# Kernel tuning notes

Hardware: AMD Instinct MI355X
Metric: run time of the kernel (lower is better)

The kernel has to match this reference:

```python
import jax, jax.numpy as jnp
import numpy as np
from jax import lax

N, E, DIN, D, L, H, T, NE = 20000, 240000, 768, 256, 3, 4, 9, 8  # nodes, edges, input_dim, gnn_dim, layers, heads, tags, n_etype
DH = D // H
BN_EPS = 1e-5

def _bn(x, g, b):
    # eval-mode BatchNorm1d with running stats (mean=0, var=1)
    return x * (g / np.sqrt(1.0 + BN_EPS)) + b

def _gelu(x):
    return jax.nn.gelu(x, approximate=False)

def setup_inputs():
    key = jax.random.key(0)
    ks = iter(jax.random.split(key, 48))
    nrm = lambda shape: jax.random.normal(next(ks), shape, jnp.float32) * 0.02
    return {
        "node_emb": jax.random.normal(next(ks), (N, DIN), jnp.float32),
        "edge_index": jax.random.randint(next(ks), (2, E), 0, N),
        "edge_type": jax.random.randint(next(ks), (E,), 0, NE),
        "tag_gt": jax.random.randint(next(ks), (N,), 0, T),
        "W_lm2gnn": nrm((DIN, D)), "b_lm2gnn": jnp.zeros((D,)),
        "We1": nrm((L, NE + 1, D)), "be1": jnp.zeros((L, D)),
        "g1": jnp.ones((L, D)), "bb1": jnp.zeros((L, D)),
        "We2": nrm((L, D, D)), "be2": jnp.zeros((L, D)),
        "Wq": nrm((L, D, D)), "bq": jnp.zeros((L, D)),
        "Wk": nrm((L, 2 * D, D)), "bk": jnp.zeros((L, D)),
        "Wm": nrm((L, 2 * D, D)), "bm": jnp.zeros((L, D)),
        "Wp1": nrm((L, D, D)), "bp1": jnp.zeros((L, D)),
        "g2": jnp.ones((L, D)), "bb2": jnp.zeros((L, D)),
        "Wp2": nrm((L, D, D)), "bp2": jnp.zeros((L, D)),
        "Wo": nrm((D, D)), "bo": jnp.zeros((D,)),
        "Wc": nrm((D, D)), "bc": jnp.zeros((D,)),
        "Wt": nrm((D, T)), "bt": jnp.zeros((T,)),
        "crf_start": nrm((T,)), "crf_end": nrm((T,)), "crf_trans": nrm((T, T)),
    }

def _emissions(node_emb, edge_index, edge_type, W_lm2gnn, b_lm2gnn, We1, be1, g1, bb1,
               We2, be2, Wq, bq, Wk, bk, Wm, bm, Wp1, bp1, g2, bb2, Wp2, bp2,
               Wo, bo, Wc, bc, Wt, bt):
    H0 = _gelu(node_emb @ W_lm2gnn + b_lm2gnn)
    loop = jnp.arange(N)
    src = jnp.concatenate([edge_index[0], loop])          # (Etot,)
    dst = jnp.concatenate([edge_index[1], loop])
    # one-hot edge types + self-loop type NE
    ev = jnp.concatenate([jax.nn.one_hot(edge_type, NE + 1, dtype=jnp.float32),
                          jnp.zeros((N, NE + 1), jnp.float32).at[:, NE].set(1.0)], axis=0)
    deg = jax.ops.segment_sum(jnp.ones_like(src, jnp.float32), src, N)[src]  # src out-degree per edge
    X = H0
    for l in range(L):
        e = _bn(ev @ We1[l] + be1[l], g1[l], bb1[l])
        e = jax.nn.relu(e) @ We2[l] + be2[l]              # edge embeddings (Etot, D)
        x_i, x_j = X[dst], X[src]                          # target, source gathers
        q = (x_j @ Wq[l] + bq[l]).reshape(-1, H, DH)
        k = (x_i @ Wk[l][:D] + e @ Wk[l][D:] + bk[l]).reshape(-1, H, DH)
        m = (x_j @ Wm[l][:D] + e @ Wm[l][D:] + bm[l]).reshape(-1, H, DH)
        s = (q * k).sum(-1) / np.sqrt(DH)                  # (Etot, H)
        smax = jax.ops.segment_max(s, src, N)[src]
        ex = jnp.exp(s - smax)
        den = jax.ops.segment_sum(ex, src, N)[src]
        alpha = ex / (den + 1e-16) * deg[:, None]          # segment softmax over src, degree-scaled
        out_e = (m * alpha[:, :, None]).reshape(-1, D)
        aggr = jax.ops.segment_sum(out_e, dst, N)          # scatter-add to targets
        Xl = _bn(aggr @ Wp1[l] + bp1[l], g2[l], bb2[l])
        X = _gelu(jax.nn.relu(Xl) @ Wp2[l] + bp2[l])       # mlp then activation (dropout = eval identity)
    hidden = _gelu((H0 @ Wo + bo) + (X @ Wc + bc))
    return hidden @ Wt + bt                                # (N, T)

def reference(node_emb, edge_index, edge_type, tag_gt, W_lm2gnn, b_lm2gnn, We1, be1, g1, bb1,
              We2, be2, Wq, bq, Wk, bk, Wm, bm, Wp1, bp1, g2, bb2, Wp2, bp2,
              Wo, bo, Wc, bc, Wt, bt, crf_start, crf_end, crf_trans):
    em = _emissions(node_emb, edge_index, edge_type, W_lm2gnn, b_lm2gnn, We1, be1, g1, bb1,
                    We2, be2, Wq, bq, Wk, bk, Wm, bm, Wp1, bp1, g2, bb2, Wp2, bp2,
                    Wo, bo, Wc, bc, Wt, bt)
    # CRF Viterbi decode (batch=1, full-length mask)
    def vstep(score, em_t):
        cand = score[:, None] + crf_trans                  # (T, T)
        return jnp.max(cand, axis=0) + em_t, jnp.argmax(cand, axis=0)
    last, bps = lax.scan(vstep, crf_start + em[0], em[1:])
    last_tag = jnp.argmax(last + crf_end)
    def back(t, bp_t):
        prev = bp_t[t]
        return prev, prev
    _, prevs = lax.scan(back, last_tag, bps, reverse=True)
    path = jnp.concatenate([prevs, last_tag[None]])
    return path[None, :]                                   # (1, N) best tag sequence
```

## Files before the change

kernel.cpp:

```cpp
#include <hip/hip_runtime.h>

#define NN 20000
#define EE 240000
#define ETOTAL 260000
#define DIN 768
#define DD 256
#define NT 9

__device__ __forceinline__ unsigned fenc(float x) {
  unsigned u = __float_as_uint(x);
  return (u & 0x80000000u) ? ~u : (u | 0x80000000u);
}
__device__ __forceinline__ float fdec(unsigned e) {
  unsigned u = (e & 0x80000000u) ? (e ^ 0x80000000u) : ~e;
  return __uint_as_float(u);
}
__device__ __forceinline__ float gelu_f(float x) {
  return 0.5f * x * (1.0f + erff(x * 0.70710678118654752440f));
}

#define VSTEP(EIN) do {                                                   \
  float f0, f1, f2, f3, f4, f5, f6, f7, f8;                               \
  float q0, q1, q2, q3, q4, q5, q6, q7, q8;                               \
  asm volatile(                                                           \
    "s_nop 1\n\t"                                                         \
    "v_readlane_b32 %[f0], %[sv], 0\n\t"                                  \
    "v_readlane_b32 %[f1], %[sv], 1\n\t"                                  \
    "v_readlane_b32 %[f2], %[sv], 2\n\t"                                  \
    "v_readlane_b32 %[f3], %[sv], 3\n\t"                                  \
    "v_readlane_b32 %[f4], %[sv], 4\n\t"                                  \
    "v_readlane_b32 %[f5], %[sv], 5\n\t"                                  \
    "v_readlane_b32 %[f6], %[sv], 6\n\t"                                  \
    "v_readlane_b32 %[f7], %[sv], 7\n\t"                                  \
    "v_readlane_b32 %[f8], %[sv], 8\n\t"                                  \
    "v_add_f32 %[q0], %[f0], %[u0]\n\t"                                   \
    "v_add_f32 %[q1], %[f1], %[u1]\n\t"                                   \
    "v_add_f32 %[q2], %[f2], %[u2]\n\t"                                   \
    "v_add_f32 %[q3], %[f3], %[u3]\n\t"                                   \
    "v_add_f32 %[q4], %[f4], %[u4]\n\t"                                   \
    "v_add_f32 %[q5], %[f5], %[u5]\n\t"                                   \
    "v_add_f32 %[q6], %[f6], %[u6]\n\t"                                   \
    "v_add_f32 %[q7], %[f7], %[u7]\n\t"                                   \
    "v_add_f32 %[q8], %[f8], %[u8]\n\t"                                   \
    "v_max3_f32 %[q0], %[q0], %[q1], %[q2]\n\t"                           \
    "v_max3_f32 %[q3], %[q3], %[q4], %[q5]\n\t"                           \
    "v_max3_f32 %[q6], %[q6], %[q7], %[q8]\n\t"                           \
    "v_max3_f32 %[q0], %[q0], %[q3], %[q6]\n\t"                           \
    "v_add_f32 %[q0], %[q0], %[e]\n\t"                                    \
    : [f0]"=&s"(f0), [f1]"=&s"(f1), [f2]"=&s"(f2),                        \
      [f3]"=&s"(f3), [f4]"=&s"(f4), [f5]"=&s"(f5),                        \
      [f6]"=&s"(f6), [f7]"=&s"(f7), [f8]"=&s"(f8),                        \
      [q0]"=&v"(q0), [q1]"=&v"(q1), [q2]"=&v"(q2),                        \
      [q3]"=&v"(q3), [q4]"=&v"(q4), [q5]"=&v"(q5),                        \
      [q6]"=&v"(q6), [q7]"=&v"(q7), [q8]"=&v"(q8)                         \
    : [sv]"v"(s), [e]"v"(EIN),                                            \
      [u0]"v"(tcol[0]), [u1]"v"(tcol[1]), [u2]"v"(tcol[2]),               \
      [u3]"v"(tcol[3]), [u4]"v"(tcol[4]), [u5]"v"(tcol[5]),               \
      [u6]"v"(tcol[6]), [u7]"v"(tcol[7]), [u8]"v"(tcol[8]));              \
  s = q0;                                                                 \
  *svp = s; svp += 64;                                                    \
} while (0)

__global__ __launch_bounds__(256) void gemm_k(
    const float* __restrict__ A, const float* __restrict__ B,
    const float* __restrict__ bias, const float* __restrict__ addc,
    const float* __restrict__ bng, const float* __restrict__ bnb,
    float* __restrict__ C, int M, int K, int N, int act)
{
  __shared__ float As[32][64];
  __shared__ float Bs[32][64];
  const int tid = threadIdx.x;
  const int tx = tid & 15, ty = tid >> 4;
  const int m0 = blockIdx.y * 64, n0 = blockIdx.x * 64;
  float acc[4][4];
#pragma unroll
  for (int i = 0; i < 4; ++i)
#pragma unroll
    for (int j = 0; j < 4; ++j) acc[i][j] = 0.f;

  for (int kk = 0; kk < K; kk += 32) {
#pragma unroll
    for (int L = tid; L < 512; L += 256) {
      int r = L >> 3, c4 = L & 7;
      int gm = m0 + r;
      float4 v = make_float4(0.f, 0.f, 0.f, 0.f);
      if (gm < M) v = *(const float4*)(A + (size_t)gm * K + kk + c4 * 4);
      As[c4 * 4 + 0][r] = v.x; As[c4 * 4 + 1][r] = v.y;
      As[c4 * 4 + 2][r] = v.z; As[c4 * 4 + 3][r] = v.w;
    }
#pragma unroll
    for (int L = tid; L < 512; L += 256) {
      int r = L >> 4, c4 = L & 15;
      *(float4*)&Bs[r][c4 * 4] = *(const float4*)(B + (size_t)(kk + r) * N + n0 + c4 * 4);
    }
    __syncthreads();
#pragma unroll
    for (int k = 0; k < 32; ++k) {
      float a[4], b[4];
      *(float4*)a = *(const float4*)&As[k][ty * 4];
      *(float4*)b = *(const float4*)&Bs[k][tx * 4];
#pragma unroll
      for (int i = 0; i < 4; ++i)
#pragma unroll
        for (int j = 0; j < 4; ++j) acc[i][j] += a[i] * b[j];
    }
    __syncthreads();
  }
  const float bnc = 0.99999500003749968752f;
#pragma unroll
  for (int i = 0; i < 4; ++i) {
    int gm = m0 + ty * 4 + i;
    if (gm >= M) continue;
    float o[4];
#pragma unroll
    for (int j = 0; j < 4; ++j) {
      int n = n0 + tx * 4 + j;
      float x = acc[i][j];
      if (bias) x += bias[n];
      if (addc) x += addc[(size_t)gm * N + n];
      if (act == 1) x = gelu_f(x);
      else if (act == 2) { x = x * (bng[n] * bnc) + bnb[n]; x = fmaxf(x, 0.f); }
      o[j] = x;
    }
    *(float4*)(C + (size_t)gm * N + n0 + tx * 4) = *(const float4*)o;
  }
}

__global__ __launch_bounds__(256) void edge_tables_k(
    const float* __restrict__ We1l, const float* __restrict__ be1l,
    const float* __restrict__ g1l, const float* __restrict__ bb1l,
    const float* __restrict__ We2l, const float* __restrict__ be2l,
    const float* __restrict__ WkEl, const float* __restrict__ bkl,
    const float* __restrict__ WmEl, const float* __restrict__ bml,
    float* __restrict__ ketab, float* __restrict__ metab)
{
  __shared__ float r_s[DD];
  __shared__ float e_s[DD];
  const int t = blockIdx.x, d = threadIdx.x;
  const float bnc = 0.99999500003749968752f;
  float pre = We1l[t * DD + d] + be1l[d];
  float bnv = pre * (g1l[d] * bnc) + bb1l[d];
  r_s[d] = fmaxf(bnv, 0.f);
  __syncthreads();
  float acc = 0.f;
  for (int c = 0; c < DD; ++c) acc += r_s[c] * We2l[c * DD + d];
  e_s[d] = acc + be2l[d];
  __syncthreads();
  float ka = 0.f, ma = 0.f;
  for (int c = 0; c < DD; ++c) {
    float ec = e_s[c];
    ka += ec * WkEl[c * DD + d];
    ma += ec * WmEl[c * DD + d];
  }
  ketab[t * DD + d] = ka + bkl[d];
  metab[t * DD + d] = ma + bml[d];
}

__global__ void deg_k(const int* __restrict__ ei, int* __restrict__ cnt,
                      int* __restrict__ cnt_d)
{
  for (int e = blockIdx.x * blockDim.x + threadIdx.x; e < EE; e += gridDim.x * blockDim.x) {
    atomicAdd(&cnt[ei[e]], 1);
    atomicAdd(&cnt_d[ei[EE + e]], 1);
  }
}

__global__ __launch_bounds__(256) void scan_k(const int* __restrict__ c,
                                              int* __restrict__ offs)
{
  __shared__ int part[257];
  const int tid = threadIdx.x;
  const int CH = (NN + 255) / 256;
  int a = tid * CH, b = a + CH; if (b > NN) b = NN;
  int s = 0;
  for (int i = a; i < b; ++i) s += c[i];
  part[tid] = s;
  __syncthreads();
  if (tid == 0) {
    int r = 0;
    for (int i = 0; i < 256; ++i) { int v = part[i]; part[i] = r; r += v; }
    part[256] = r;
  }
  __syncthreads();
  int r = part[tid];
  for (int i = a; i < b; ++i) { offs[i] = r; r += c[i]; }
  if (tid == 255) offs[NN] = part[256];
}

__global__ void fill_k(const int* __restrict__ ei, const int* __restrict__ offs,
                       int* __restrict__ fc, int* __restrict__ eix)
{
  for (int e = blockIdx.x * blockDim.x + threadIdx.x; e < EE; e += gridDim.x * blockDim.x) {
    int d = ei[EE + e];
    int p = offs[d] + atomicAdd(&fc[d], 1);
    eix[p] = e;
  }
}

__global__ __launch_bounds__(256) void score_k(
    const float* __restrict__ Q, const float* __restrict__ Kn,
    const float* __restrict__ ketab, const int* __restrict__ ei,
    const int* __restrict__ et, float* __restrict__ sbuf,
    unsigned* __restrict__ smax)
{
  __shared__ float ke_s[NT * DD];
  for (int i = threadIdx.x; i < NT * DD; i += 256) ke_s[i] = ketab[i];
  __syncthreads();
  const int lane = threadIdx.x & 63, wave = threadIdx.x >> 6;
  const float4* Q4 = (const float4*)Q;
  const float4* K4 = (const float4*)Kn;
  for (int e = blockIdx.x * 4 + wave; e < ETOTAL; e += gridDim.x * 4) {
    int src, dst, t;
    if (e < EE) { src = ei[e]; dst = ei[EE + e]; t = et[e]; }
    else { src = dst = e - EE; t = NT - 1; }
    float4 q = Q4[src * 64 + lane];
    float4 k = K4[dst * 64 + lane];
    float4 ke = *(const float4*)(ke_s + t * DD + lane * 4);
    float p = q.x * (k.x + ke.x) + q.y * (k.y + ke.y) +
              q.z * (k.z + ke.z) + q.w * (k.w + ke.w);
    p += __shfl_xor(p, 8); p += __shfl_xor(p, 4);
    p += __shfl_xor(p, 2); p += __shfl_xor(p, 1);
    if ((lane & 15) == 0) {
      int h = lane >> 4;
      float s = p * 0.125f;
      sbuf[e * 4 + h] = s;
      atomicMax(smax + src * 4 + h, fenc(s));
    }
  }
}

__global__ void softmax_k(const int* __restrict__ ei, float* __restrict__ sbuf,
                          const unsigned* __restrict__ smax, float* __restrict__ den)
{
  for (int idx = blockIdx.x * blockDim.x + threadIdx.x; idx < ETOTAL * 4;
       idx += gridDim.x * blockDim.x) {
    int e = idx >> 2, h = idx & 3;
    int src = (e < EE) ? ei[e] : e - EE;
    float s = sbuf[idx];
    float ex = expf(s - fdec(smax[src * 4 + h]));
    sbuf[idx] = ex;
    atomicAdd(den + src * 4 + h, ex);
  }
}

__global__ __launch_bounds__(256) void aggr2_k(
    const float* __restrict__ Mn, const float* __restrict__ metab,
    const int* __restrict__ ei, const int* __restrict__ et,
    const float* __restrict__ sbuf, const float* __restrict__ den,
    const int* __restrict__ cnt, const int* __restrict__ offs,
    const int* __restrict__ eix, float* __restrict__ aggr)
{
  __shared__ float me_s[NT * DD];
  for (int i = threadIdx.x; i < NT * DD; i += 256) me_s[i] = metab[i];
  __syncthreads();
  const int lane = threadIdx.x & 63, wave = threadIdx.x >> 6;
  const int h = lane >> 4;
  const float4* M4 = (const float4*)Mn;
  int dst = blockIdx.x * 4 + wave;
  if (dst >= NN) return;
  float4 acc;
  {
    float ex = sbuf[(EE + dst) * 4 + h];
    float dn = den[dst * 4 + h];
    float alpha = ex / (dn + 1e-16f) * (float)(cnt[dst] + 1);
    float4 m = M4[dst * 64 + lane];
    float4 me = *(const float4*)(me_s + (NT - 1) * DD + lane * 4);
    acc.x = (m.x + me.x) * alpha; acc.y = (m.y + me.y) * alpha;
    acc.z = (m.z + me.z) * alpha; acc.w = (m.w + me.w) * alpha;
  }
  int o1 = offs[dst + 1];
  for (int o = offs[dst]; o < o1; ++o) {
    int e = eix[o];
    int src = ei[e], t = et[e];
    float ex = sbuf[e * 4 + h];
    float dn = den[src * 4 + h];
    float alpha = ex / (dn + 1e-16f) * (float)(cnt[src] + 1);
    float4 m = M4[src * 64 + lane];
    float4 me = *(const float4*)(me_s + t * DD + lane * 4);
    acc.x += (m.x + me.x) * alpha; acc.y += (m.y + me.y) * alpha;
    acc.z += (m.z + me.z) * alpha; acc.w += (m.w + me.w) * alpha;
  }
  ((float4*)aggr)[dst * 64 + lane] = acc;
}

__global__ __launch_bounds__(256) void emis_k(
    const float* __restrict__ hidden, const float* __restrict__ Wt,
    const float* __restrict__ bt, float* __restrict__ em)
{
  __shared__ float wt_s[DD * NT];
  for (int i = threadIdx.x; i < DD * NT; i += 256) wt_s[i] = Wt[i];
  __syncthreads();
  const int lane = threadIdx.x & 63, wave = threadIdx.x >> 6;
  const float4* H4 = (const float4*)hidden;
  for (int n = blockIdx.x * 4 + wave; n < NN; n += gridDim.x * 4) {
    float4 h = H4[n * 64 + lane];
    const float* w0 = wt_s + (lane * 4) * NT;
    float p[NT];
#pragma unroll
    for (int t = 0; t < NT; ++t)
      p[t] = h.x * w0[t] + h.y * w0[NT + t] + h.z * w0[2 * NT + t] + h.w * w0[3 * NT + t];
#pragma unroll
    for (int m = 32; m >= 1; m >>= 1)
#pragma unroll
      for (int t = 0; t < NT; ++t) p[t] += __shfl_xor(p[t], m);
    if (lane == 0) {
#pragma unroll
      for (int t = 0; t < NT; ++t) em[n * NT + t] = p[t] + bt[t];
    }
  }
}

__global__ __launch_bounds__(256) void viterbi_k(
    const float* __restrict__ em, const float* __restrict__ cstart,
    const float* __restrict__ cend, const float* __restrict__ ctrans,
    float* __restrict__ sv, int* __restrict__ outp)
{
  const int VCS = 512;
  const int NCH = (NN + VCS - 1) / VCS;
  __shared__ float embuf[2][VCS * NT + 32];
  __shared__ float trT[NT * 16];
  __shared__ float scf[NT];
  __shared__ unsigned char fmaps[256][NT];
  __shared__ unsigned char ends_s[256];
  __shared__ int last_s;
  const int tid = threadIdx.x, lane = tid & 63, wave = tid >> 6;
  const int jl = min(lane & 15, NT - 1);

  for (int i = tid; i < VCS * NT; i += 256) embuf[0][i] = em[i];
  if (tid < NT * NT) trT[(tid % NT) * 16 + (tid / NT)] = ctrans[tid];
  __syncthreads();

  float tcol[NT];
  float s = 0.f;
  if (wave == 0) {
#pragma unroll
    for (int i = 0; i < NT; ++i) tcol[i] = ctrans[i * NT + jl];
    s = cstart[jl] + embuf[0][jl];
    sv[lane] = s;
  }

  for (int c = 0; c < NCH; ++c) {
    if (wave > 0) {
      if (c + 1 < NCH) {
        int base = (c + 1) * VCS * NT;
        int n2 = VCS * NT;
        if (base + n2 > NN * NT) n2 = NN * NT - base;
        for (int i = tid - 64; i < n2; i += 192) embuf[(c + 1) & 1][i] = em[base + i];
      }
    } else {
      const float* eb = embuf[c & 1];
      int tbeg = (c == 0) ? 1 : c * VCS;
      int tend = (c + 1) * VCS; if (tend > NN) tend = NN;
      int off = tbeg - c * VCS;
      int nsteps = tend - tbeg;
      float* svp = sv + (size_t)tbeg * 64 + lane;
      int i = 0;
      if (nsteps >= 12) {
        float a0 = eb[(off + 0) * NT + jl], a1 = eb[(off + 1) * NT + jl];
        float a2 = eb[(off + 2) * NT + jl], a3 = eb[(off + 3) * NT + jl];
        float b0 = eb[(off + 4) * NT + jl], b1 = eb[(off + 5) * NT + jl];
        float b2 = eb[(off + 6) * NT + jl], b3 = eb[(off + 7) * NT + jl];
        int nblk = (nsteps - 8) / 4;
        for (int bk = 0; bk < nblk; ++bk) {
          int lo = off + 8 + bk * 4;
          float n0 = eb[(lo + 0) * NT + jl];
          float n1 = eb[(lo + 1) * NT + jl];
          float n2v = eb[(lo + 2) * NT + jl];
          float n3 = eb[(lo + 3) * NT + jl];
          VSTEP(a0); VSTEP(a1); VSTEP(a2); VSTEP(a3);
          a0 = b0; a1 = b1; a2 = b2; a3 = b3;
          b0 = n0; b1 = n1; b2 = n2v; b3 = n3;
        }
        i = nblk * 4;
        VSTEP(a0); VSTEP(a1); VSTEP(a2); VSTEP(a3);
        VSTEP(b0); VSTEP(b1); VSTEP(b2); VSTEP(b3);
        i += 8;
      }
      for (; i < nsteps; ++i) {
        float e0 = eb[(off + i) * NT + jl];
        VSTEP(e0);
      }
    }
    __syncthreads();
  }

  if (wave == 0 && lane < NT) scf[lane] = s + cend[lane];
  __syncthreads();
  if (tid == 0) {
    float bv = scf[0]; int bi = 0;
    for (int j = 1; j < NT; ++j) if (scf[j] > bv) { bv = scf[j]; bi = j; }
    last_s = bi;
  }
  __syncthreads();

  const int RL = 79;
  int a = 1 + tid * RL;
  int b = a + RL; if (b > NN) b = NN;
  bool active = (a < NN);
  if (active) {
    int x[NT];
#pragma unroll
    for (int j = 0; j < NT; ++j) x[j] = j;
    for (int t = b - 1; t >= a; --t) {
      const float* sp = sv + (size_t)(t - 1) * 64;
      float sr[NT];
#pragma unroll
      for (int i = 0; i < NT; ++i) sr[i] = sp[i];
#pragma unroll
      for (int j = 0; j < NT; ++j) {
        const float* tcx = trT + x[j] * 16;
        float bv = sr[0] + tcx[0]; int bi = 0;
#pragma unroll
        for (int i = 1; i < NT; ++i) {
          float cv = sr[i] + tcx[i];
          if (cv > bv) { bv = cv; bi = i; }
        }
        x[j] = bi;
      }
    }
#pragma unroll
    for (int j = 0; j < NT; ++j) fmaps[tid][j] = (unsigned char)x[j];
  }
  __syncthreads();
  if (tid == 0) {
    int x = last_s;
    for (int k = 255; k >= 0; --k) {
      ends_s[k] = (unsigned char)x;
      int ak = 1 + k * RL;
      if (ak < NN) x = fmaps[k][x];
    }
  }
  __syncthreads();
  if (active) {
    int x = ends_s[tid];
    outp[b - 1] = x;
    for (int t = b - 1; t >= a; --t) {
      const float* sp = sv + (size_t)(t - 1) * 64;
      const float* tcx = trT + x * 16;
      float bv = sp[0] + tcx[0]; int bi = 0;
#pragma unroll
      for (int i = 1; i < NT; ++i) {
        float cv = sp[i] + tcx[i];
        if (cv > bv) { bv = cv; bi = i; }
      }
      x = bi;
      outp[t - 1] = x;
    }
  }
}

extern "C" void kernel_launch(void* const* d_in, const int* in_sizes, int n_in,
                              void* d_out, int out_size, void* d_ws, size_t ws_size,
                              hipStream_t stream)
{
  const float* node_emb = (const float*)d_in[0];
  const int* edge_index = (const int*)d_in[1];
  const int* edge_type = (const int*)d_in[2];
  const float* W_lm2gnn = (const float*)d_in[4];
  const float* b_lm2gnn = (const float*)d_in[5];
  const float* We1 = (const float*)d_in[6];
  const float* be1 = (const float*)d_in[7];
  const float* g1 = (const float*)d_in[8];
  const float* bb1 = (const float*)d_in[9];
  const float* We2 = (const float*)d_in[10];
  const float* be2 = (const float*)d_in[11];
  const float* Wq = (const float*)d_in[12];
  const float* bq = (const float*)d_in[13];
  const float* Wk = (const float*)d_in[14];
  const float* bk = (const float*)d_in[15];
  const float* Wm = (const float*)d_in[16];
  const float* bm = (const float*)d_in[17];
  const float* Wp1 = (const float*)d_in[18];
  const float* bp1 = (const float*)d_in[19];
  const float* g2 = (const float*)d_in[20];
  const float* bb2 = (const float*)d_in[21];
  const float* Wp2 = (const float*)d_in[22];
  const float* bp2 = (const float*)d_in[23];
  const float* Wo = (const float*)d_in[24];
  const float* bo = (const float*)d_in[25];
  const float* Wc = (const float*)d_in[26];
  const float* bc = (const float*)d_in[27];
  const float* Wt = (const float*)d_in[28];
  const float* bt = (const float*)d_in[29];
  const float* cstart = (const float*)d_in[30];
  const float* cend = (const float*)d_in[31];
  const float* ctrans = (const float*)d_in[32];

  const size_t NB = (size_t)NN * DD * sizeof(float);
  char* w = (char*)d_ws;
  float* H0 = (float*)(w + 0 * NB);
  float* Xb = (float*)(w + 1 * NB);
  float* Qb = (float*)(w + 2 * NB);
  float* Kb = (float*)(w + 3 * NB);
  char* sm = w + 4 * NB;
  size_t smo = 0;
  auto alloc = [&](size_t bytes) { char* p = sm + smo; smo += (bytes + 255) & ~255ull; return p; };
  float* sbuf = (float*)alloc((size_t)ETOTAL * 4 * 4);
  unsigned* smax = (unsigned*)alloc((size_t)NN * 4 * 4);
  float* den = (float*)alloc((size_t)NN * 4 * 4);
  int* cnt = (int*)alloc((size_t)NN * 4);
  int* cnt_d = (int*)alloc((size_t)NN * 4);
  int* offs = (int*)alloc((size_t)(NN + 1) * 4);
  int* fc = (int*)alloc((size_t)NN * 4);
  int* eix = (int*)alloc((size_t)EE * 4);
  float* ketab = (float*)alloc((size_t)NT * DD * 4);
  float* metab = (float*)alloc((size_t)NT * DD * 4);
  float* em = (float*)alloc((size_t)NN * NT * 4);
  float* sv = (float*)alloc(((size_t)NN * 64 + 64) * 4);
  const size_t needed = 4 * NB + smo;
  if (ws_size < needed) return;

  dim3 gg(DD / 64, (NN + 63) / 64);

  hipMemsetAsync(cnt, 0, (size_t)((char*)eix - (char*)cnt), stream);
  deg_k<<<1024, 256, 0, stream>>>(edge_index, cnt, cnt_d);
  scan_k<<<1, 256, 0, stream>>>(cnt_d, offs);
  fill_k<<<1024, 256, 0, stream>>>(edge_index, offs, fc, eix);

  gemm_k<<<gg, 256, 0, stream>>>(node_emb, W_lm2gnn, b_lm2gnn, nullptr, nullptr,
                                 nullptr, H0, NN, DIN, DD, 1);

  const float* Xcur = H0;
  for (int l = 0; l < 3; ++l) {
    edge_tables_k<<<NT, 256, 0, stream>>>(
        We1 + (size_t)l * NT * DD, be1 + l * DD, g1 + l * DD, bb1 + l * DD,
        We2 + (size_t)l * DD * DD, be2 + l * DD,
        Wk + (size_t)l * 2 * DD * DD + DD * DD, bk + l * DD,
        Wm + (size_t)l * 2 * DD * DD + DD * DD, bm + l * DD, ketab, metab);

    gemm_k<<<gg, 256, 0, stream>>>(Xcur, Wq + (size_t)l * DD * DD, bq + l * DD,
                                   nullptr, nullptr, nullptr, Qb, NN, DD, DD, 0);
    gemm_k<<<gg, 256, 0, stream>>>(Xcur, Wk + (size_t)l * 2 * DD * DD, nullptr,
                                   nullptr, nullptr, nullptr, Kb, NN, DD, DD, 0);

    hipMemsetAsync(smax, 0, (size_t)NN * 4 * 4 * 2, stream);
    score_k<<<2048, 256, 0, stream>>>(Qb, Kb, ketab, edge_index, edge_type, sbuf, smax);
    softmax_k<<<2048, 256, 0, stream>>>(edge_index, sbuf, smax, den);

    gemm_k<<<gg, 256, 0, stream>>>(Xcur, Wm + (size_t)l * 2 * DD * DD, nullptr,
                                   nullptr, nullptr, nullptr, Qb, NN, DD, DD, 0);
    aggr2_k<<<(NN + 3) / 4, 256, 0, stream>>>(Qb, metab, edge_index, edge_type,
                                              sbuf, den, cnt, offs, eix, Kb);

    gemm_k<<<gg, 256, 0, stream>>>(Kb, Wp1 + (size_t)l * DD * DD, bp1 + l * DD,
                                   nullptr, g2 + l * DD, bb2 + l * DD, Qb, NN, DD, DD, 2);
    gemm_k<<<gg, 256, 0, stream>>>(Qb, Wp2 + (size_t)l * DD * DD, bp2 + l * DD,
                                   nullptr, nullptr, nullptr, Xb, NN, DD, DD, 1);
    Xcur = Xb;
  }

  gemm_k<<<gg, 256, 0, stream>>>(H0, Wo, bo, nullptr, nullptr, nullptr, Kb, NN, DD, DD, 0);
  gemm_k<<<gg, 256, 0, stream>>>(Xb, Wc, bc, Kb, nullptr, nullptr, Qb, NN, DD, DD, 1);

  emis_k<<<1250, 256, 0, stream>>>(Qb, Wt, bt, em);
  viterbi_k<<<1, 256, 0, stream>>>(em, cstart, cend, ctrans, sv, (int*)d_out);
}
```

Before: 3.085 ms.

## Fuse Q/K/M projection GEMMs and concatenate final output GEMMs

New measurement: 2.931 ms. 1.05x faster.

```diff
diff --git a/kernel.cpp b/kernel.cpp
--- a/kernel.cpp
+++ b/kernel.cpp
@@ -63,7 +63,7 @@
 
 __global__ __launch_bounds__(256) void gemm_k(
     const float* __restrict__ A, const float* __restrict__ B,
-    const float* __restrict__ bias, const float* __restrict__ addc,
+    const float* __restrict__ bias,
     const float* __restrict__ bng, const float* __restrict__ bnb,
     float* __restrict__ C, int M, int K, int N, int act)
 {
@@ -117,12 +117,144 @@
       int n = n0 + tx * 4 + j;
       float x = acc[i][j];
       if (bias) x += bias[n];
-      if (addc) x += addc[(size_t)gm * N + n];
       if (act == 1) x = gelu_f(x);
       else if (act == 2) { x = x * (bng[n] * bnc) + bnb[n]; x = fmaxf(x, 0.f); }
       o[j] = x;
     }
     *(float4*)(C + (size_t)gm * N + n0 + tx * 4) = *(const float4*)o;
+  }
+}
+
+__global__ __launch_bounds__(256) void gemm3_k(
+    const float* __restrict__ A, const float* __restrict__ B0,
+    const float* __restrict__ bias0, const float* __restrict__ B1,
+    const float* __restrict__ B2, float* __restrict__ C0,
+    float* __restrict__ C1, float* __restrict__ C2, int M)
+{
+  __shared__ float As[32][64];
+  __shared__ float Bs[3][32][64];
+  const int tid = threadIdx.x;
+  const int tx = tid & 15, ty = tid >> 4;
+  const int m0 = blockIdx.y * 64, n0 = blockIdx.x * 64;
+  float acc0[4][4], acc1[4][4], acc2[4][4];
+#pragma unroll
+  for (int i = 0; i < 4; ++i)
+#pragma unroll
+    for (int j = 0; j < 4; ++j) { acc0[i][j] = 0.f; acc1[i][j] = 0.f; acc2[i][j] = 0.f; }
+
+  for (int kk = 0; kk < DD; kk += 32) {
+#pragma unroll
+    for (int L = tid; L < 512; L += 256) {
+      int r = L >> 3, c4 = L & 7;
+      int gm = m0 + r;
+      float4 v = make_float4(0.f, 0.f, 0.f, 0.f);
+      if (gm < M) v = *(const float4*)(A + (size_t)gm * DD + kk + c4 * 4);
+      As[c4 * 4 + 0][r] = v.x; As[c4 * 4 + 1][r] = v.y;
+      As[c4 * 4 + 2][r] = v.z; As[c4 * 4 + 3][r] = v.w;
+    }
+#pragma unroll
+    for (int L = tid; L < 1536; L += 256) {
+      int which = L >> 9, r = (L >> 4) & 31, c4 = L & 15;
+      const float* Bp = (which == 0) ? B0 : (which == 1) ? B1 : B2;
+      *(float4*)&Bs[which][r][c4 * 4] =
+          *(const float4*)(Bp + (size_t)(kk + r) * DD + n0 + c4 * 4);
+    }
+    __syncthreads();
+#pragma unroll
+    for (int k = 0; k < 32; ++k) {
+      float a[4], b0[4], b1[4], b2[4];
+      *(float4*)a = *(const float4*)&As[k][ty * 4];
+      *(float4*)b0 = *(const float4*)&Bs[0][k][tx * 4];
+      *(float4*)b1 = *(const float4*)&Bs[1][k][tx * 4];
+      *(float4*)b2 = *(const float4*)&Bs[2][k][tx * 4];
+#pragma unroll
+      for (int i = 0; i < 4; ++i)
+#pragma unroll
+        for (int j = 0; j < 4; ++j) {
+          acc0[i][j] += a[i] * b0[j];
+          acc1[i][j] += a[i] * b1[j];
+          acc2[i][j] += a[i] * b2[j];
+        }
+    }
+    __syncthreads();
+  }
+#pragma unroll
+  for (int i = 0; i < 4; ++i) {
+    int gm = m0 + ty * 4 + i;
+    if (gm >= M) continue;
+    float o0[4], o1[4], o2[4];
+#pragma unroll
+    for (int j = 0; j < 4; ++j) {
+      int n = n0 + tx * 4 + j;
+      o0[j] = acc0[i][j] + bias0[n];
+      o1[j] = acc1[i][j];
+      o2[j] = acc2[i][j];
+    }
+    *(float4*)(C0 + (size_t)gm * DD + n0 + tx * 4) = *(const float4*)o0;
+    *(float4*)(C1 + (size_t)gm * DD + n0 + tx * 4) = *(const float4*)o1;
+    *(float4*)(C2 + (size_t)gm * DD + n0 + tx * 4) = *(const float4*)o2;
+  }
+}
+
+__global__ __launch_bounds__(256) void gemm_cat_k(
+    const float* __restrict__ A1, const float* __restrict__ B1,
+    const float* __restrict__ bias1, const float* __restrict__ A2,
+    const float* __restrict__ B2, const float* __restrict__ bias2,
+    float* __restrict__ C, int M)
+{
+  __shared__ float As[32][64];
+  __shared__ float Bs[32][64];
+  const int tid = threadIdx.x;
+  const int tx = tid & 15, ty = tid >> 4;
+  const int m0 = blockIdx.y * 64, n0 = blockIdx.x * 64;
+  float acc[4][4];
+#pragma unroll
+  for (int i = 0; i < 4; ++i)
+#pragma unroll
+    for (int j = 0; j < 4; ++j) acc[i][j] = 0.f;
+
+  for (int kk = 0; kk < 2 * DD; kk += 32) {
+    const float* Ap = (kk < DD) ? A1 : A2;
+    const float* Bp = (kk < DD) ? B1 : B2;
+    const int ko = kk & (DD - 1);
+#pragma unroll
+    for (int L = tid; L < 512; L += 256) {
+      int r = L >> 3, c4 = L & 7;
+      int gm = m0 + r;
+      float4 v = make_float4(0.f, 0.f, 0.f, 0.f);
+      if (gm < M) v = *(const float4*)(Ap + (size_t)gm * DD + ko + c4 * 4);
+      As[c4 * 4 + 0][r] = v.x; As[c4 * 4 + 1][r] = v.y;
+      As[c4 * 4 + 2][r] = v.z; As[c4 * 4 + 3][r] = v.w;
+    }
+#pragma unroll
+    for (int L = tid; L < 512; L += 256) {
+      int r = L >> 4, c4 = L & 15;
+      *(float4*)&Bs[r][c4 * 4] = *(const float4*)(Bp + (size_t)(ko + r) * DD + n0 + c4 * 4);
+    }
+    __syncthreads();
+#pragma unroll
+    for (int k = 0; k < 32; ++k) {
+      float a[4], b[4];
+      *(float4*)a = *(const float4*)&As[k][ty * 4];
+      *(float4*)b = *(const float4*)&Bs[k][tx * 4];
+#pragma unroll
+      for (int i = 0; i < 4; ++i)
+#pragma unroll
+        for (int j = 0; j < 4; ++j) acc[i][j] += a[i] * b[j];
+    }
+    __syncthreads();
+  }
+#pragma unroll
+  for (int i = 0; i < 4; ++i) {
+    int gm = m0 + ty * 4 + i;
+    if (gm >= M) continue;
+    float o[4];
+#pragma unroll
+    for (int j = 0; j < 4; ++j) {
+      int n = n0 + tx * 4 + j;
+      o[j] = gelu_f(acc[i][j] + bias1[n] + bias2[n]);
+    }
+    *(float4*)(C + (size_t)gm * DD + n0 + tx * 4) = *(const float4*)o;
   }
 }
 
@@ -492,7 +624,8 @@
   float* Xb = (float*)(w + 1 * NB);
   float* Qb = (float*)(w + 2 * NB);
   float* Kb = (float*)(w + 3 * NB);
-  char* sm = w + 4 * NB;
+  float* Mb = (float*)(w + 4 * NB);
+  char* sm = w + 5 * NB;
   size_t smo = 0;
   auto alloc = [&](size_t bytes) { char* p = sm + smo; smo += (bytes + 255) & ~255ull; return p; };
   float* sbuf = (float*)alloc((size_t)ETOTAL * 4 * 4);
@@ -507,7 +640,7 @@
   float* metab = (float*)alloc((size_t)NT * DD * 4);
   float* em = (float*)alloc((size_t)NN * NT * 4);
   float* sv = (float*)alloc(((size_t)NN * 64 + 64) * 4);
-  const size_t needed = 4 * NB + smo;
+  const size_t needed = 5 * NB + smo;
   if (ws_size < needed) return;
 
   dim3 gg(DD / 64, (NN + 63) / 64);
@@ -517,7 +650,7 @@
   scan_k<<<1, 256, 0, stream>>>(cnt_d, offs);
   fill_k<<<1024, 256, 0, stream>>>(edge_index, offs, fc, eix);
 
-  gemm_k<<<gg, 256, 0, stream>>>(node_emb, W_lm2gnn, b_lm2gnn, nullptr, nullptr,
+  gemm_k<<<gg, 256, 0, stream>>>(node_emb, W_lm2gnn, b_lm2gnn, nullptr,
                                  nullptr, H0, NN, DIN, DD, 1);
 
   const float* Xcur = H0;
@@ -528,29 +661,26 @@
         Wk + (size_t)l * 2 * DD * DD + DD * DD, bk + l * DD,
         Wm + (size_t)l * 2 * DD * DD + DD * DD, bm + l * DD, ketab, metab);
 
-    gemm_k<<<gg, 256, 0, stream>>>(Xcur, Wq + (size_t)l * DD * DD, bq + l * DD,
-                                   nullptr, nullptr, nullptr, Qb, NN, DD, DD, 0);
-    gemm_k<<<gg, 256, 0, stream>>>(Xcur, Wk + (size_t)l * 2 * DD * DD, nullptr,
-                                   nullptr, nullptr, nullptr, Kb, NN, DD, DD, 0);
+    gemm3_k<<<gg, 256, 0, stream>>>(Xcur, Wq + (size_t)l * DD * DD, bq + l * DD,
+                                    Wk + (size_t)l * 2 * DD * DD,
+                                    Wm + (size_t)l * 2 * DD * DD,
+                                    Qb, Kb, Mb, NN);
 
     hipMemsetAsync(smax, 0, (size_t)NN * 4 * 4 * 2, stream);
     score_k<<<2048, 256, 0, stream>>>(Qb, Kb, ketab, edge_index, edge_type, sbuf, smax);
     softmax_k<<<2048, 256, 0, stream>>>(edge_index, sbuf, smax, den);
 
-    gemm_k<<<gg, 256, 0, stream>>>(Xcur, Wm + (size_t)l * 2 * DD * DD, nullptr,
-                                   nullptr, nullptr, nullptr, Qb, NN, DD, DD, 0);
-    aggr2_k<<<(NN + 3) / 4, 256, 0, stream>>>(Qb, metab, edge_index, edge_type,
+    aggr2_k<<<(NN + 3) / 4, 256, 0, stream>>>(Mb, metab, edge_index, edge_type,
                                               sbuf, den, cnt, offs, eix, Kb);
 
     gemm_k<<<gg, 256, 0, stream>>>(Kb, Wp1 + (size_t)l * DD * DD, bp1 + l * DD,
-                                   nullptr, g2 + l * DD, bb2 + l * DD, Qb, NN, DD, DD, 2);
+                                   g2 + l * DD, bb2 + l * DD, Qb, NN, DD, DD, 2);
     gemm_k<<<gg, 256, 0, stream>>>(Qb, Wp2 + (size_t)l * DD * DD, bp2 + l * DD,
-                                   nullptr, nullptr, nullptr, Xb, NN, DD, DD, 1);
+                                   nullptr, nullptr, Xb, NN, DD, DD, 1);
     Xcur = Xb;
   }
 
-  gemm_k<<<gg, 256, 0, stream>>>(H0, Wo, bo, nullptr, nullptr, nullptr, Kb, NN, DD, DD, 0);
-  gemm_k<<<gg, 256, 0, stream>>>(Xb, Wc, bc, Kb, nullptr, nullptr, Qb, NN, DD, DD, 1);
+  gemm_cat_k<<<gg, 256, 0, stream>>>(H0, Wo, bo, Xb, Wc, bc, Qb, NN);
 
   emis_k<<<1250, 256, 0, stream>>>(Qb, Wt, bt, em);
   viterbi_k<<<1, 256, 0, stream>>>(em, cstart, cend, ctrans, sv, (int*)d_out);
```
